# Performance work log

Hardware: AMD Instinct MI355X
Metric: run time of the kernel (lower is better)

Reference implementation:

```python
import jax, jax.numpy as jnp
import numpy as np

EPS = 1.1920929e-07  # torch.finfo(float32).eps, used by nn.RMSNorm when eps=None
H = 16  # num_heads


def rmsnorm(x, w):
    return x * jax.lax.rsqrt(jnp.mean(x * x, axis=-1, keepdims=True) + EPS) * w


def attention(x, wq, wk, wv, wo, mask):
    # x: [b, s, d]; mask: [s, s] bool (True = attend)
    b, s, d = x.shape
    hd = d // H
    split = lambda t: t.reshape(b, s, H, hd).transpose(0, 2, 1, 3)  # b h s hd
    q, k, v = split(x @ wq), split(x @ wk), split(x @ wv)
    scale = 1.0 / float(np.sqrt(hd))
    scores = jnp.einsum('bhqd,bhkd->bhqk', q, k) * scale
    scores = jnp.where(mask, scores, jnp.asarray(-1e30, scores.dtype))
    p = jax.nn.softmax(scores, axis=-1)
    o = jnp.einsum('bhqk,bhkd->bhqd', p, v)
    return o.transpose(0, 2, 1, 3).reshape(b, s, d) @ wo


def setup_inputs() -> dict:
    key = jax.random.key(0)
    B, S, D, DFF = 2, 1024, 1024, 4096
    ks = jax.random.split(key, 32)
    w = lambda k, shape: jax.random.normal(k, shape, jnp.float32) * 0.02

    idx = jnp.arange(S)
    col_id = idx % 32            # COLUMN: interleaved column groups
    feat_id = idx // 128         # FEATURE: contiguous feature groups
    col_mask = col_id[:, None] == col_id[None, :]
    feat_mask = feat_id[:, None] == feat_id[None, :]
    nbr_mask = jnp.abs(idx[:, None] - idx[None, :]) <= 64  # NEIGHBOR: local band
    full_mask = jnp.ones((S, S), dtype=bool)

    return {
        'x': jax.random.normal(ks[0], (B, S, D), jnp.float32),
        'col_mask': col_mask, 'feat_mask': feat_mask,
        'nbr_mask': nbr_mask, 'full_mask': full_mask,
        'norm_c': jnp.ones((D,), jnp.float32), 'wq_c': w(ks[1], (D, D)), 'wk_c': w(ks[2], (D, D)), 'wv_c': w(ks[3], (D, D)), 'wo_c': w(ks[4], (D, D)),
        'norm_f': jnp.ones((D,), jnp.float32), 'wq_f': w(ks[5], (D, D)), 'wk_f': w(ks[6], (D, D)), 'wv_f': w(ks[7], (D, D)), 'wo_f': w(ks[8], (D, D)),
        'norm_n': jnp.ones((D,), jnp.float32), 'wq_n': w(ks[9], (D, D)), 'wk_n': w(ks[10], (D, D)), 'wv_n': w(ks[11], (D, D)), 'wo_n': w(ks[12], (D, D)),
        'norm_u': jnp.ones((D,), jnp.float32), 'wq_u': w(ks[13], (D, D)), 'wk_u': w(ks[14], (D, D)), 'wv_u': w(ks[15], (D, D)), 'wo_u': w(ks[16], (D, D)),
        'norm_ffn': jnp.ones((D,), jnp.float32), 'w_up': w(ks[17], (D, DFF)), 'w_gate': w(ks[18], (D, DFF)), 'w_down': w(ks[19], (DFF, D)),
    }


def reference(x, col_mask, feat_mask, nbr_mask, full_mask,
              norm_c, wq_c, wk_c, wv_c, wo_c,
              norm_f, wq_f, wk_f, wv_f, wo_f,
              norm_n, wq_n, wk_n, wv_n, wo_n,
              norm_u, wq_u, wk_u, wv_u, wo_u,
              norm_ffn, w_up, w_gate, w_down):
    x = x + attention(rmsnorm(x, norm_c), wq_c, wk_c, wv_c, wo_c, col_mask)
    x = x + attention(rmsnorm(x, norm_f), wq_f, wk_f, wv_f, wo_f, feat_mask)
    x = x + attention(rmsnorm(x, norm_n), wq_n, wk_n, wv_n, wo_n, nbr_mask)
    x = x + attention(rmsnorm(x, norm_u), wq_u, wk_u, wv_u, wo_u, full_mask)
    h = rmsnorm(x, norm_ffn)
    x = x + (jax.nn.silu(h @ w_gate) * (h @ w_up)) @ w_down  # SwiGLU FFN
    return x
```

## Files before the change

### kernel.cpp

```cpp
#include <hip/hip_runtime.h>
#include <math.h>
#include <stdint.h>


typedef __attribute__((ext_vector_type(8))) short bf16x8;
typedef __attribute__((ext_vector_type(4))) float f32x4;
typedef unsigned short ushort_t;
typedef unsigned int uint_t;

#define DEV static __device__ __forceinline__

DEV float bf2f(ushort_t u) { union { uint_t i; float f; } v; v.i = ((uint_t)u) << 16; return v.f; }
DEV ushort_t f2bf(float f) {
  union { float f; uint_t i; } v; v.f = f;
  uint_t r = v.i + 0x7fffu + ((v.i >> 16) & 1u);
  return (ushort_t)(r >> 16);
}
DEV uint_t pk2(ushort_t a, ushort_t b) { return (uint_t)a | ((uint_t)b << 16); }

DEV void gld16(const ushort_t* g, ushort_t* l) {
  __builtin_amdgcn_global_load_lds((const __attribute__((address_space(1))) void*)g,
                                   (__attribute__((address_space(3))) void*)l, 16, 0, 0);
}

struct Src16 { const float* p[16]; };

__global__ __launch_bounds__(256) void transpose16(Src16 s, ushort_t* __restrict__ qkvT,
                                                   ushort_t* __restrict__ woT) {
  __shared__ float tile[32][33];
  const int mz = blockIdx.z;
  const float* __restrict__ src = s.p[mz];
  const int l = mz >> 2, which = mz & 3;
  ushort_t* dst = (which < 3) ? (qkvT + (size_t)l*3072*1024 + (size_t)which*1024*1024)
                              : (woT  + (size_t)l*1024*1024);
  const int tx = threadIdx.x & 31, ty = threadIdx.x >> 5;
  const int r0 = blockIdx.y*32, c0 = blockIdx.x*32;
#pragma unroll
  for (int i = 0; i < 4; i++) tile[ty + 8*i][tx] = src[(size_t)(r0 + ty + 8*i)*1024 + c0 + tx];
  __syncthreads();
#pragma unroll
  for (int i = 0; i < 4; i++) dst[(size_t)(c0 + ty + 8*i)*1024 + r0 + tx] = f2bf(tile[tx][ty + 8*i]);
}

__global__ __launch_bounds__(256) void transpose_cvt(const float* __restrict__ src,
    ushort_t* __restrict__ dst, int R, int C, int row_off) {
  __shared__ float tile[32][33];
  const int tx = threadIdx.x & 31, ty = threadIdx.x >> 5;
  const int r0 = blockIdx.y*32, c0 = blockIdx.x*32;
#pragma unroll
  for (int i = 0; i < 4; i++) tile[ty + 8*i][tx] = src[(size_t)(r0 + ty + 8*i)*C + c0 + tx];
  __syncthreads();
#pragma unroll
  for (int i = 0; i < 4; i++)
    dst[(size_t)(row_off + c0 + ty + 8*i)*R + r0 + tx] = f2bf(tile[tx][ty + 8*i]);
}

__global__ __launch_bounds__(256) void copy_f32(const float* __restrict__ src,
                                                float* __restrict__ dst) {
  const size_t i = (size_t)blockIdx.x*256 + threadIdx.x;
  ((float4*)dst)[i] = ((const float4*)src)[i];
}

__global__ __launch_bounds__(256) void rmsnorm_k(const float* __restrict__ x,
    const float* __restrict__ w, ushort_t* __restrict__ out) {
  const int row = blockIdx.x, t = threadIdx.x;
  const float4 v = ((const float4*)(x + (size_t)row*1024))[t];
  float ss = v.x*v.x + v.y*v.y + v.z*v.z + v.w*v.w;
#pragma unroll
  for (int m = 32; m; m >>= 1) ss += __shfl_xor(ss, m);
  __shared__ float red[4];
  if ((t & 63) == 0) red[t >> 6] = ss;
  __syncthreads();
  const float tot = red[0] + red[1] + red[2] + red[3];
  const float rs = rsqrtf(tot * (1.0f/1024.0f) + 1.1920929e-07f);
  const float4 wv = ((const float4*)w)[t];
  uint2 o;
  o.x = pk2(f2bf(v.x*rs*wv.x), f2bf(v.y*rs*wv.y));
  o.y = pk2(f2bf(v.z*rs*wv.z), f2bf(v.w*rs*wv.w));
  *(uint2*)&out[(size_t)row*1024 + t*4] = o;
}

template<int BM, int BN, int EPI, int SPLITK>
__global__ __launch_bounds__(256, 2) void gemm_bt(
    const ushort_t* __restrict__ A, const ushort_t* __restrict__ BT,
    void* __restrict__ Cout, int M, int N, int K) {
  constexpr int BK = 64;
  __shared__ ushort_t Al[BM*BK];
  __shared__ ushort_t Bl[BN*BK];
  const int t = threadIdx.x, lane = t & 63;
  const int l15 = lane & 15, l4 = lane >> 4;
  int bid = blockIdx.y * gridDim.x + blockIdx.x;
  const int nwg = gridDim.x * gridDim.y;
  if ((nwg & 7) == 0) bid = (bid & 7) * (nwg >> 3) + (bid >> 3);
  const int n0 = (bid % gridDim.x) * BN;
  const int m0 = (bid / gridDim.x) * BM;
  constexpr int WM = BM/2, WN = BN/2, FM = WM/16, FN = WN/16;
  const int wm = ((t >> 6) >> 1) * WM;
  const int wn = ((t >> 6) & 1) * WN;
  const f32x4 zf = {0.f, 0.f, 0.f, 0.f};
  f32x4 acc[FM][FN];
#pragma unroll
  for (int m = 0; m < FM; m++)
#pragma unroll
    for (int n = 0; n < FN; n++) acc[m][n] = zf;
  constexpr int CA = (BM*BK)/(256*8), CB = (BN*BK)/(256*8);
  const int kz = blockIdx.z * (K / SPLITK);
  for (int k0 = kz; k0 < kz + K / SPLITK; k0 += BK) {
#pragma unroll
    for (int i = 0; i < CA; i++) {
      const int c = i*256 + t;
      gld16(&A[(size_t)(m0 + (c >> 3))*K + k0 + (c & 7)*8], &Al[c*8]);
    }
#pragma unroll
    for (int i = 0; i < CB; i++) {
      const int c = i*256 + t;
      gld16(&BT[(size_t)(n0 + (c >> 3))*K + k0 + (c & 7)*8], &Bl[c*8]);
    }
    __syncthreads();
#pragma unroll
    for (int kc = 0; kc < BK; kc += 32) {
      bf16x8 af[FM], bfr[FN];
#pragma unroll
      for (int m = 0; m < FM; m++) af[m] = *(const bf16x8*)&Al[(wm + m*16 + l15)*BK + kc + l4*8];
#pragma unroll
      for (int n = 0; n < FN; n++) bfr[n] = *(const bf16x8*)&Bl[(wn + n*16 + l15)*BK + kc + l4*8];
#pragma unroll
      for (int m = 0; m < FM; m++)
#pragma unroll
        for (int n = 0; n < FN; n++)
          acc[m][n] = __builtin_amdgcn_mfma_f32_16x16x32_bf16(af[m], bfr[n], acc[m][n], 0, 0, 0);
    }
    __syncthreads();
  }
#pragma unroll
  for (int m = 0; m < FM; m++)
#pragma unroll
    for (int n = 0; n < FN; n++)
#pragma unroll
      for (int r = 0; r < 4; r++) {
        const int row = m0 + wm + m*16 + l4*4 + r;
        const int col = n0 + wn + n*16 + l15;
        const size_t idx = (size_t)row*N + col;
        const float v = acc[m][n][r];
        if (EPI == 0) ((ushort_t*)Cout)[idx] = f2bf(v);
        else          atomicAdd(&((float*)Cout)[idx], v);
      }
}

__global__ __launch_bounds__(256) void attn_col_k(const ushort_t* __restrict__ qkv,
                                                  ushort_t* __restrict__ O) {
  __shared__ float Qs[32][65], Ks[32][65], Vs[32][65], P[32][33];
  const int c = blockIdx.x, h = blockIdx.y, b = blockIdx.z, t = threadIdx.x;
  const size_t base = (size_t)b*1024*3072 + h*64;
  for (int e = t; e < 2048; e += 256) {
    const int u = e >> 6, d = e & 63;
    const size_t rb = base + (size_t)(c + 32*u)*3072 + d;
    Qs[u][d] = bf2f(qkv[rb]);
    Ks[u][d] = bf2f(qkv[rb + 1024]);
    Vs[u][d] = bf2f(qkv[rb + 2048]);
  }
  __syncthreads();
  const int u = t >> 3, kq = (t & 7)*4;
  float sc[4] = {0.f, 0.f, 0.f, 0.f};
  for (int d = 0; d < 64; d++) {
    const float q = Qs[u][d];
#pragma unroll
    for (int j = 0; j < 4; j++) sc[j] += q * Ks[kq + j][d];
  }
#pragma unroll
  for (int j = 0; j < 4; j++) P[u][kq + j] = sc[j] * 0.125f;
  __syncthreads();
  if (t < 32) {
    float mx = P[t][0];
    for (int j = 1; j < 32; j++) mx = fmaxf(mx, P[t][j]);
    float sum = 0.f;
    for (int j = 0; j < 32; j++) { const float p = __expf(P[t][j] - mx); P[t][j] = p; sum += p; }
    const float inv = 1.0f / sum;
    for (int j = 0; j < 32; j++) P[t][j] *= inv;
  }
  __syncthreads();
  const int dg = (t & 7)*8;
  float o[8] = {0.f,0.f,0.f,0.f,0.f,0.f,0.f,0.f};
  for (int k = 0; k < 32; k++) {
    const float p = P[u][k];
#pragma unroll
    for (int j = 0; j < 8; j++) o[j] += p * Vs[k][dg + j];
  }
  uint4 w4;
  w4.x = pk2(f2bf(o[0]), f2bf(o[1])); w4.y = pk2(f2bf(o[2]), f2bf(o[3]));
  w4.z = pk2(f2bf(o[4]), f2bf(o[5])); w4.w = pk2(f2bf(o[6]), f2bf(o[7]));
  *(uint4*)&O[(size_t)(b*1024 + c + 32*u)*1024 + h*64 + dg] = w4;
}

template<int MASK>
__global__ __launch_bounds__(256) void attn_flash_k(const ushort_t* __restrict__ qkv,
                                                    ushort_t* __restrict__ O) {
  constexpr int KP = 72, VP = 40, PP = 40;
  __shared__ ushort_t Kl[32*KP];
  __shared__ ushort_t Vtl[64*VP];
  __shared__ ushort_t Pl[4][16*PP];
  const int t = threadIdx.x, lane = t & 63, wave = t >> 6;
  const int l15 = lane & 15, l4 = lane >> 4;
  const int qt = blockIdx.x, h = blockIdx.y, b = blockIdx.z;
  const int q0 = qt*64;
  const size_t base = (size_t)b*1024*3072 + h*64;
  const int qrow = q0 + wave*16 + l15;
  const bf16x8 qf0 = *(const bf16x8*)&qkv[base + (size_t)qrow*3072 + l4*8];
  const bf16x8 qf1 = *(const bf16x8*)&qkv[base + (size_t)qrow*3072 + 32 + l4*8];
  int klo, khi;
  if (MASK == 0)      { klo = q0 & ~127; khi = klo + 128; }
  else if (MASK == 1) { klo = (q0 >= 64) ? q0 - 64 : 0; khi = (q0 + 128 < 1024) ? q0 + 128 : 1024; }
  else                { klo = 0; khi = 1024; }
  const f32x4 zf = {0.f, 0.f, 0.f, 0.f};
  f32x4 of[4];
#pragma unroll
  for (int n = 0; n < 4; n++) of[n] = zf;
  float mrow[4], lrow[4];
#pragma unroll
  for (int r = 0; r < 4; r++) { mrow[r] = -INFINITY; lrow[r] = 0.f; }
  const int skrow = t >> 3, sdb = (t & 7)*8;

  for (int kb = klo; kb < khi; kb += 32) {
    {
      const size_t rb = base + (size_t)(kb + skrow)*3072 + sdb;
      const bf16x8 kv = *(const bf16x8*)&qkv[rb + 1024];
      const bf16x8 vv = *(const bf16x8*)&qkv[rb + 2048];
      *(bf16x8*)&Kl[skrow*KP + sdb] = kv;
#pragma unroll
      for (int j = 0; j < 8; j++) Vtl[(sdb + j)*VP + skrow] = (ushort_t)vv[j];
    }
    __syncthreads();
    f32x4 sf0 = zf, sf1 = zf;
    {
      const bf16x8 k00 = *(const bf16x8*)&Kl[(l15)*KP + l4*8];
      const bf16x8 k01 = *(const bf16x8*)&Kl[(l15)*KP + 32 + l4*8];
      const bf16x8 k10 = *(const bf16x8*)&Kl[(16 + l15)*KP + l4*8];
      const bf16x8 k11 = *(const bf16x8*)&Kl[(16 + l15)*KP + 32 + l4*8];
      sf0 = __builtin_amdgcn_mfma_f32_16x16x32_bf16(qf0, k00, sf0, 0, 0, 0);
      sf0 = __builtin_amdgcn_mfma_f32_16x16x32_bf16(qf1, k01, sf0, 0, 0, 0);
      sf1 = __builtin_amdgcn_mfma_f32_16x16x32_bf16(qf0, k10, sf1, 0, 0, 0);
      sf1 = __builtin_amdgcn_mfma_f32_16x16x32_bf16(qf1, k11, sf1, 0, 0, 0);
    }
    float s0[4], s1[4], tmax[4];
#pragma unroll
    for (int r = 0; r < 4; r++) {
      float a = sf0[r]*0.125f, bb = sf1[r]*0.125f;
      if (MASK == 1) {
        const int qg = q0 + wave*16 + l4*4 + r;
        const int d0 = qg - (kb + l15), d1 = qg - (kb + 16 + l15);
        if (d0 > 64 || d0 < -64) a = -INFINITY;
        if (d1 > 64 || d1 < -64) bb = -INFINITY;
      }
      s0[r] = a; s1[r] = bb;
      tmax[r] = fmaxf(a, bb);
    }
#pragma unroll
    for (int mk = 1; mk < 16; mk <<= 1)
#pragma unroll
      for (int r = 0; r < 4; r++) tmax[r] = fmaxf(tmax[r], __shfl_xor(tmax[r], mk));
    float fac[4], psum[4];
#pragma unroll
    for (int r = 0; r < 4; r++) {
      const float mn = fmaxf(mrow[r], tmax[r]);
      float p0, p1;
      if (mn == -INFINITY) { fac[r] = 1.0f; p0 = 0.f; p1 = 0.f; }
      else {
        fac[r] = __expf(mrow[r] - mn);
        p0 = __expf(s0[r] - mn); p1 = __expf(s1[r] - mn);
        mrow[r] = mn;
      }
      psum[r] = p0 + p1;
      Pl[wave][(l4*4 + r)*PP + l15]      = f2bf(p0);
      Pl[wave][(l4*4 + r)*PP + 16 + l15] = f2bf(p1);
    }
#pragma unroll
    for (int mk = 1; mk < 16; mk <<= 1)
#pragma unroll
      for (int r = 0; r < 4; r++) psum[r] += __shfl_xor(psum[r], mk);
#pragma unroll
    for (int r = 0; r < 4; r++) lrow[r] = lrow[r]*fac[r] + psum[r];
#pragma unroll
    for (int n = 0; n < 4; n++)
#pragma unroll
      for (int r = 0; r < 4; r++) of[n][r] *= fac[r];
    const bf16x8 pa = *(const bf16x8*)&Pl[wave][l15*PP + l4*8];
#pragma unroll
    for (int n = 0; n < 4; n++) {
      const bf16x8 vf = *(const bf16x8*)&Vtl[(n*16 + l15)*VP + l4*8];
      of[n] = __builtin_amdgcn_mfma_f32_16x16x32_bf16(pa, vf, of[n], 0, 0, 0);
    }
    __syncthreads();
  }
#pragma unroll
  for (int n = 0; n < 4; n++)
#pragma unroll
    for (int r = 0; r < 4; r++) {
      const int qg = q0 + wave*16 + l4*4 + r;
      O[(size_t)(b*1024 + qg)*1024 + h*64 + n*16 + l15] = f2bf(of[n][r] / lrow[r]);
    }
}

__global__ __launch_bounds__(256) void swiglu_k(const ushort_t* __restrict__ gu,
                                                ushort_t* __restrict__ out) {
  const size_t idx = (size_t)blockIdx.x*256 + threadIdx.x;
  const size_t m = idx >> 9, j8 = (idx & 511) << 3;
  const bf16x8 g8 = *(const bf16x8*)&gu[m*8192 + j8];
  const bf16x8 u8 = *(const bf16x8*)&gu[m*8192 + 4096 + j8];
  ushort_t o[8];
#pragma unroll
  for (int i = 0; i < 8; i++) {
    const float g = bf2f((ushort_t)g8[i]);
    const float u = bf2f((ushort_t)u8[i]);
    o[i] = f2bf(u * g / (1.0f + __expf(-g)));
  }
  uint4 w4;
  w4.x = pk2(o[0], o[1]); w4.y = pk2(o[2], o[3]); w4.z = pk2(o[4], o[5]); w4.w = pk2(o[6], o[7]);
  *(uint4*)&out[m*4096 + j8] = w4;
}

extern "C" void kernel_launch(void* const* d_in, const int* in_sizes, int n_in,
                              void* d_out, int out_size, void* d_ws, size_t ws_size,
                              hipStream_t stream) {
  (void)in_sizes; (void)n_in; (void)out_size; (void)ws_size;
  const float* x_in = (const float*)d_in[0];
  const float* norm[5] = { (const float*)d_in[5], (const float*)d_in[10], (const float*)d_in[15],
                           (const float*)d_in[20], (const float*)d_in[25] };
  char* w = (char*)d_ws;
  auto alloc = [&](size_t bytes) { char* p = w; w += (bytes + 255) & ~(size_t)255; return p; };
  ushort_t* qkvT = (ushort_t*)alloc(4ull*3072*1024*2);
  ushort_t* woT  = (ushort_t*)alloc(4ull*1024*1024*2);
  ushort_t* guT  = (ushort_t*)alloc(8192ull*1024*2);
  ushort_t* dnT  = (ushort_t*)alloc(4096ull*1024*2);
  float*    xbuf = (float*)  alloc(2048ull*1024*4);
  ushort_t* xn   = (ushort_t*)alloc(2048ull*1024*2);
  ushort_t* qkv  = (ushort_t*)alloc(2048ull*3072*2);
  ushort_t* attO = (ushort_t*)alloc(2048ull*1024*2);
  ushort_t* gu   = (ushort_t*)alloc(2048ull*8192*2);
  ushort_t* hmid = (ushort_t*)alloc(2048ull*4096*2);

  Src16 s;
  for (int l = 0; l < 4; l++) {
    s.p[l*4 + 0] = (const float*)d_in[6 + l*5];
    s.p[l*4 + 1] = (const float*)d_in[7 + l*5];
    s.p[l*4 + 2] = (const float*)d_in[8 + l*5];
    s.p[l*4 + 3] = (const float*)d_in[9 + l*5];
  }
  transpose16<<<dim3(32, 32, 16), 256, 0, stream>>>(s, qkvT, woT);
  transpose_cvt<<<dim3(128, 32), 256, 0, stream>>>((const float*)d_in[27], guT, 1024, 4096, 0);
  transpose_cvt<<<dim3(128, 32), 256, 0, stream>>>((const float*)d_in[26], guT, 1024, 4096, 4096);
  transpose_cvt<<<dim3(32, 128), 256, 0, stream>>>((const float*)d_in[28], dnT, 4096, 1024, 0);

  copy_f32<<<2048, 256, 0, stream>>>(x_in, xbuf);

  for (int l = 0; l < 4; l++) {
    rmsnorm_k<<<2048, 256, 0, stream>>>(xbuf, norm[l], xn);
    gemm_bt<64,128,0,1><<<dim3(3072/128, 2048/64), 256, 0, stream>>>(
        xn, qkvT + (size_t)l*3072*1024, qkv, 2048, 3072, 1024);
    if (l == 0)      attn_col_k        <<<dim3(32, 16, 2), 256, 0, stream>>>(qkv, attO);
    else if (l == 1) attn_flash_k<0>   <<<dim3(16, 16, 2), 256, 0, stream>>>(qkv, attO);
    else if (l == 2) attn_flash_k<1>   <<<dim3(16, 16, 2), 256, 0, stream>>>(qkv, attO);
    else             attn_flash_k<2>   <<<dim3(16, 16, 2), 256, 0, stream>>>(qkv, attO);
    gemm_bt<64,64,2,2><<<dim3(1024/64, 2048/64, 2), 256, 0, stream>>>(
        attO, woT + (size_t)l*1024*1024, xbuf, 2048, 1024, 1024);
  }
  rmsnorm_k<<<2048, 256, 0, stream>>>(xbuf, norm[4], xn);
  gemm_bt<128,128,0,1><<<dim3(8192/128, 2048/128), 256, 0, stream>>>(xn, guT, gu, 2048, 8192, 1024);
  swiglu_k<<<4096, 256, 0, stream>>>(gu, hmid);
  copy_f32<<<2048, 256, 0, stream>>>(xbuf, (float*)d_out);
  gemm_bt<64,64,2,4><<<dim3(1024/64, 2048/64, 4), 256, 0, stream>>>(
      hmid, dnT, d_out, 2048, 1024, 4096);
}
```

Before: 617.5 us.

## Split full-attention KV range across blocks with merge kernel, widen KV tile

```diff
diff --git a/kernel.cpp b/kernel.cpp
--- a/kernel.cpp
+++ b/kernel.cpp
@@ -192,16 +192,17 @@
   *(uint4*)&O[(size_t)(b*1024 + c + 32*u)*1024 + h*64 + dg] = w4;
 }
 
-template<int MASK>
+template<int MASK, int NSPLIT>
 __global__ __launch_bounds__(256) void attn_flash_k(const ushort_t* __restrict__ qkv,
-                                                    ushort_t* __restrict__ O) {
-  constexpr int KP = 72, VP = 40, PP = 40;
-  __shared__ ushort_t Kl[32*KP];
-  __shared__ ushort_t Vtl[64*VP];
-  __shared__ ushort_t Pl[4][16*PP];
+    ushort_t* __restrict__ O, float* __restrict__ Opart, float* __restrict__ MLpart) {
+  constexpr int LP = 66;
+  __shared__ ushort_t Kl[64*LP];
+  __shared__ ushort_t Vt[64*LP];
+  __shared__ ushort_t Pl[4][16*LP];
   const int t = threadIdx.x, lane = t & 63, wave = t >> 6;
   const int l15 = lane & 15, l4 = lane >> 4;
-  const int qt = blockIdx.x, h = blockIdx.y, b = blockIdx.z;
+  const int qt = blockIdx.x, h = blockIdx.y;
+  const int b = blockIdx.z / NSPLIT, sp = blockIdx.z % NSPLIT;
   const int q0 = qt*64;
   const size_t base = (size_t)b*1024*3072 + h*64;
   const int qrow = q0 + wave*16 + l15;
@@ -210,7 +211,15 @@
   int klo, khi;
   if (MASK == 0)      { klo = q0 & ~127; khi = klo + 128; }
   else if (MASK == 1) { klo = (q0 >= 64) ? q0 - 64 : 0; khi = (q0 + 128 < 1024) ? q0 + 128 : 1024; }
-  else                { klo = 0; khi = 1024; }
+  else                { klo = sp * (1024/NSPLIT); khi = klo + 1024/NSPLIT; }
+  const int kr = t >> 2, kd = (t & 3)*16;
+  const int vk = lane,  vd = wave*16;
+  const ushort_t* kptr = qkv + base + 1024 + (size_t)kr*3072 + kd;
+  const ushort_t* vptr = qkv + base + 2048 + (size_t)vk*3072 + vd;
+  bf16x8 kg0 = *(const bf16x8*)&kptr[(size_t)klo*3072];
+  bf16x8 kg1 = *(const bf16x8*)&kptr[(size_t)klo*3072 + 8];
+  bf16x8 vg0 = *(const bf16x8*)&vptr[(size_t)klo*3072];
+  bf16x8 vg1 = *(const bf16x8*)&vptr[(size_t)klo*3072 + 8];
   const f32x4 zf = {0.f, 0.f, 0.f, 0.f};
   f32x4 of[4];
 #pragma unroll
@@ -218,42 +227,46 @@
   float mrow[4], lrow[4];
 #pragma unroll
   for (int r = 0; r < 4; r++) { mrow[r] = -INFINITY; lrow[r] = 0.f; }
-  const int skrow = t >> 3, sdb = (t & 7)*8;
-
-  for (int kb = klo; kb < khi; kb += 32) {
-    {
-      const size_t rb = base + (size_t)(kb + skrow)*3072 + sdb;
-      const bf16x8 kv = *(const bf16x8*)&qkv[rb + 1024];
-      const bf16x8 vv = *(const bf16x8*)&qkv[rb + 2048];
-      *(bf16x8*)&Kl[skrow*KP + sdb] = kv;
-#pragma unroll
-      for (int j = 0; j < 8; j++) Vtl[(sdb + j)*VP + skrow] = (ushort_t)vv[j];
-    }
+
+  for (int kb = klo; kb < khi; kb += 64) {
+    *(bf16x8*)&Kl[kr*LP + kd] = kg0;
+    *(bf16x8*)&Kl[kr*LP + kd + 8] = kg1;
+#pragma unroll
+    for (int j = 0; j < 8; j++) Vt[(vd + j)*LP + vk] = (ushort_t)vg0[j];
+#pragma unroll
+    for (int j = 0; j < 8; j++) Vt[(vd + 8 + j)*LP + vk] = (ushort_t)vg1[j];
     __syncthreads();
-    f32x4 sf0 = zf, sf1 = zf;
-    {
-      const bf16x8 k00 = *(const bf16x8*)&Kl[(l15)*KP + l4*8];
-      const bf16x8 k01 = *(const bf16x8*)&Kl[(l15)*KP + 32 + l4*8];
-      const bf16x8 k10 = *(const bf16x8*)&Kl[(16 + l15)*KP + l4*8];
-      const bf16x8 k11 = *(const bf16x8*)&Kl[(16 + l15)*KP + 32 + l4*8];
-      sf0 = __builtin_amdgcn_mfma_f32_16x16x32_bf16(qf0, k00, sf0, 0, 0, 0);
-      sf0 = __builtin_amdgcn_mfma_f32_16x16x32_bf16(qf1, k01, sf0, 0, 0, 0);
-      sf1 = __builtin_amdgcn_mfma_f32_16x16x32_bf16(qf0, k10, sf1, 0, 0, 0);
-      sf1 = __builtin_amdgcn_mfma_f32_16x16x32_bf16(qf1, k11, sf1, 0, 0, 0);
-    }
-    float s0[4], s1[4], tmax[4];
-#pragma unroll
-    for (int r = 0; r < 4; r++) {
-      float a = sf0[r]*0.125f, bb = sf1[r]*0.125f;
-      if (MASK == 1) {
-        const int qg = q0 + wave*16 + l4*4 + r;
-        const int d0 = qg - (kb + l15), d1 = qg - (kb + 16 + l15);
-        if (d0 > 64 || d0 < -64) a = -INFINITY;
-        if (d1 > 64 || d1 < -64) bb = -INFINITY;
+    if (kb + 64 < khi) {
+      kg0 = *(const bf16x8*)&kptr[(size_t)(kb+64)*3072];
+      kg1 = *(const bf16x8*)&kptr[(size_t)(kb+64)*3072 + 8];
+      vg0 = *(const bf16x8*)&vptr[(size_t)(kb+64)*3072];
+      vg1 = *(const bf16x8*)&vptr[(size_t)(kb+64)*3072 + 8];
+    }
+    f32x4 sf[4];
+    __builtin_amdgcn_s_setprio(1);
+#pragma unroll
+    for (int s = 0; s < 4; s++) {
+      const bf16x8 k0 = *(const bf16x8*)&Kl[(s*16 + l15)*LP + l4*8];
+      const bf16x8 k1 = *(const bf16x8*)&Kl[(s*16 + l15)*LP + 32 + l4*8];
+      sf[s] = __builtin_amdgcn_mfma_f32_16x16x32_bf16(qf0, k0, zf, 0, 0, 0);
+      sf[s] = __builtin_amdgcn_mfma_f32_16x16x32_bf16(qf1, k1, sf[s], 0, 0, 0);
+    }
+    __builtin_amdgcn_s_setprio(0);
+    float sv[4][4], tmax[4];
+#pragma unroll
+    for (int r = 0; r < 4; r++) tmax[r] = -INFINITY;
+#pragma unroll
+    for (int s = 0; s < 4; s++)
+#pragma unroll
+      for (int r = 0; r < 4; r++) {
+        float a = sf[s][r]*0.125f;
+        if (MASK == 1) {
+          const int d = (q0 + wave*16 + l4*4 + r) - (kb + s*16 + l15);
+          if (d > 64 || d < -64) a = -INFINITY;
+        }
+        sv[s][r] = a;
+        tmax[r] = fmaxf(tmax[r], a);
       }
-      s0[r] = a; s1[r] = bb;
-      tmax[r] = fmaxf(a, bb);
-    }
 #pragma unroll
     for (int mk = 1; mk < 16; mk <<= 1)
 #pragma unroll
@@ -262,16 +275,23 @@
 #pragma unroll
     for (int r = 0; r < 4; r++) {
       const float mn = fmaxf(mrow[r], tmax[r]);
-      float p0, p1;
-      if (mn == -INFINITY) { fac[r] = 1.0f; p0 = 0.f; p1 = 0.f; }
-      else {
+      psum[r] = 0.f;
+      if (mn == -INFINITY) {
+        fac[r] = 1.0f;
+#pragma unroll
+        for (int s = 0; s < 4; s++) {
+          Pl[wave][(l4*4 + r)*LP + s*16 + l15] = 0;
+        }
+      } else {
         fac[r] = __expf(mrow[r] - mn);
-        p0 = __expf(s0[r] - mn); p1 = __expf(s1[r] - mn);
         mrow[r] = mn;
+#pragma unroll
+        for (int s = 0; s < 4; s++) {
+          const float p = __expf(sv[s][r] - mn);
+          psum[r] += p;
+          Pl[wave][(l4*4 + r)*LP + s*16 + l15] = f2bf(p);
+        }
       }
-      psum[r] = p0 + p1;
-      Pl[wave][(l4*4 + r)*PP + l15]      = f2bf(p0);
-      Pl[wave][(l4*4 + r)*PP + 16 + l15] = f2bf(p1);
     }
 #pragma unroll
     for (int mk = 1; mk < 16; mk <<= 1)
@@ -283,21 +303,68 @@
     for (int n = 0; n < 4; n++)
 #pragma unroll
       for (int r = 0; r < 4; r++) of[n][r] *= fac[r];
-    const bf16x8 pa = *(const bf16x8*)&Pl[wave][l15*PP + l4*8];
+    const bf16x8 pa0 = *(const bf16x8*)&Pl[wave][l15*LP + l4*8];
+    const bf16x8 pa1 = *(const bf16x8*)&Pl[wave][l15*LP + 32 + l4*8];
+    __builtin_amdgcn_s_setprio(1);
 #pragma unroll
     for (int n = 0; n < 4; n++) {
-      const bf16x8 vf = *(const bf16x8*)&Vtl[(n*16 + l15)*VP + l4*8];
-      of[n] = __builtin_amdgcn_mfma_f32_16x16x32_bf16(pa, vf, of[n], 0, 0, 0);
-    }
+      const bf16x8 v0 = *(const bf16x8*)&Vt[(n*16 + l15)*LP + l4*8];
+      const bf16x8 v1 = *(const bf16x8*)&Vt[(n*16 + l15)*LP + 32 + l4*8];
+      of[n] = __builtin_amdgcn_mfma_f32_16x16x32_bf16(pa0, v0, of[n], 0, 0, 0);
+      of[n] = __builtin_amdgcn_mfma_f32_16x16x32_bf16(pa1, v1, of[n], 0, 0, 0);
+    }
+    __builtin_amdgcn_s_setprio(0);
     __syncthreads();
   }
-#pragma unroll
-  for (int n = 0; n < 4; n++)
+  if (NSPLIT == 1) {
+#pragma unroll
+    for (int n = 0; n < 4; n++)
+#pragma unroll
+      for (int r = 0; r < 4; r++) {
+        const int qg = q0 + wave*16 + l4*4 + r;
+        O[(size_t)(b*1024 + qg)*1024 + h*64 + n*16 + l15] = f2bf(of[n][r] / lrow[r]);
+      }
+  } else {
 #pragma unroll
     for (int r = 0; r < 4; r++) {
       const int qg = q0 + wave*16 + l4*4 + r;
-      O[(size_t)(b*1024 + qg)*1024 + h*64 + n*16 + l15] = f2bf(of[n][r] / lrow[r]);
-    }
+      const size_t row = ((size_t)(sp*2 + b)*1024 + qg)*16 + h;
+#pragma unroll
+      for (int n = 0; n < 4; n++) Opart[row*64 + n*16 + l15] = of[n][r];
+      if (l15 == 0) *(float2*)&MLpart[row*2] = make_float2(mrow[r], lrow[r]);
+    }
+  }
+}
+
+__global__ __launch_bounds__(256) void attn_merge_k(const float* __restrict__ Opart,
+    const float* __restrict__ ML, ushort_t* __restrict__ O) {
+  const int idx = blockIdx.x*256 + threadIdx.x;
+  const int d8 = (idx & 7)*8;
+  const int h  = (idx >> 3) & 15;
+  const int q  = (idx >> 7) & 1023;
+  const int b  = idx >> 17;
+  const size_t r0 = ((size_t)b*1024 + q)*16 + h;
+  const size_t r1 = ((size_t)(2 + b)*1024 + q)*16 + h;
+  const float2 ml0 = *(const float2*)&ML[r0*2];
+  const float2 ml1 = *(const float2*)&ML[r1*2];
+  const float m = fmaxf(ml0.x, ml1.x);
+  const float w0 = __expf(ml0.x - m), w1 = __expf(ml1.x - m);
+  const float inv = 1.0f / (ml0.y*w0 + ml1.y*w1);
+  const float4* o0 = (const float4*)&Opart[r0*64 + d8];
+  const float4* o1 = (const float4*)&Opart[r1*64 + d8];
+  ushort_t ob[8];
+#pragma unroll
+  for (int i = 0; i < 2; i++) {
+    const float4 a = o0[i], c = o1[i];
+    ob[i*4+0] = f2bf((a.x*w0 + c.x*w1)*inv);
+    ob[i*4+1] = f2bf((a.y*w0 + c.y*w1)*inv);
+    ob[i*4+2] = f2bf((a.z*w0 + c.z*w1)*inv);
+    ob[i*4+3] = f2bf((a.w*w0 + c.w*w1)*inv);
+  }
+  uint4 w4;
+  w4.x = pk2(ob[0], ob[1]); w4.y = pk2(ob[2], ob[3]);
+  w4.z = pk2(ob[4], ob[5]); w4.w = pk2(ob[6], ob[7]);
+  *(uint4*)&O[((size_t)b*1024 + q)*1024 + h*64 + d8] = w4;
 }
 
 __global__ __launch_bounds__(256) void swiglu_k(const ushort_t* __restrict__ gu,
@@ -337,6 +404,8 @@
   ushort_t* attO = (ushort_t*)alloc(2048ull*1024*2);
   ushort_t* gu   = (ushort_t*)alloc(2048ull*8192*2);
   ushort_t* hmid = (ushort_t*)alloc(2048ull*4096*2);
+  float* Opart  = (float*)gu;
+  float* MLpart = (float*)hmid;
 
   Src16 s;
   for (int l = 0; l < 4; l++) {
@@ -356,10 +425,13 @@
     rmsnorm_k<<<2048, 256, 0, stream>>>(xbuf, norm[l], xn);
     gemm_bt<64,128,0,1><<<dim3(3072/128, 2048/64), 256, 0, stream>>>(
         xn, qkvT + (size_t)l*3072*1024, qkv, 2048, 3072, 1024);
-    if (l == 0)      attn_col_k        <<<dim3(32, 16, 2), 256, 0, stream>>>(qkv, attO);
-    else if (l == 1) attn_flash_k<0>   <<<dim3(16, 16, 2), 256, 0, stream>>>(qkv, attO);
-    else if (l == 2) attn_flash_k<1>   <<<dim3(16, 16, 2), 256, 0, stream>>>(qkv, attO);
-    else             attn_flash_k<2>   <<<dim3(16, 16, 2), 256, 0, stream>>>(qkv, attO);
+    if (l == 0)      attn_col_k         <<<dim3(32, 16, 2), 256, 0, stream>>>(qkv, attO);
+    else if (l == 1) attn_flash_k<0,1>  <<<dim3(16, 16, 2), 256, 0, stream>>>(qkv, attO, nullptr, nullptr);
+    else if (l == 2) attn_flash_k<1,1>  <<<dim3(16, 16, 2), 256, 0, stream>>>(qkv, attO, nullptr, nullptr);
+    else {
+      attn_flash_k<2,2><<<dim3(16, 16, 4), 256, 0, stream>>>(qkv, nullptr, Opart, MLpart);
+      attn_merge_k<<<1024, 256, 0, stream>>>(Opart, MLpart, attO);
+    }
     gemm_bt<64,64,2,2><<<dim3(1024/64, 2048/64, 2), 256, 0, stream>>>(
         attO, woT + (size_t)l*1024*1024, xbuf, 2048, 1024, 1024);
   }
```

Result: faster. 600.2 us (-2.8%).
